# Kernel optimization log

Measured on AMD Instinct MI355X. Metric: run time of the kernel, lower is better.

The kernel has to match this reference:

```python
import jax, jax.numpy as jnp
from jax import lax
import numpy as np

T, C_IN, H, W = 32, 64, 128, 128
C_OUT, KH, KW = 128, 5, 5
H_OUT, W_OUT = H - KH + 1, W - KW + 1  # 124, 124
K_WINNERS = 256
LR_PLUS, LR_MINUS = 0.004, -0.003
LOWER, UPPER = 0.0, 1.0


def setup_inputs() -> dict:
    key = jax.random.key(0)
    k1, k2, k3, k4, k5, k6 = jax.random.split(key, 6)
    input_spikes = (jax.random.uniform(k1, (T, C_IN, H, W)) < 0.1).astype(jnp.float32)
    output_spikes = (jax.random.uniform(k2, (T, C_OUT, H_OUT, W_OUT)) < 0.05).astype(jnp.float32)
    weight = jax.random.uniform(k3, (C_OUT, C_IN, KH, KW), dtype=jnp.float32)
    f = jax.random.randint(k4, (K_WINNERS,), 0, C_OUT, dtype=jnp.int32)
    r = jax.random.randint(k5, (K_WINNERS,), 0, H_OUT, dtype=jnp.int32)
    c = jax.random.randint(k6, (K_WINNERS,), 0, W_OUT, dtype=jnp.int32)
    winners = jnp.stack([f, r, c], axis=1)  # [K, 3]
    return {"input_spikes": input_spikes, "output_spikes": output_spikes,
            "weight": weight, "winners": winners}


def reference(input_spikes, output_spikes, weight, winners):
    # latencies: sum spikes over time
    in_lat = jnp.sum(input_spikes, axis=0)    # [C_in, H, W]
    out_lat = jnp.sum(output_spikes, axis=0)  # [C_out, H_out, W_out]

    # gather per-winner input patches [K, C_in, kh, kw]
    def patch(rc):
        return lax.dynamic_slice(in_lat, (0, rc[0], rc[1]), (C_IN, KH, KW))
    patches = jax.vmap(patch)(winners[:, 1:])

    out_vals = out_lat[winners[:, 0], winners[:, 1], winners[:, 2]]  # [K]
    pair = patches >= out_vals[:, None, None, None]                  # [K, C_in, kh, kw]
    lr_vals = jnp.where(pair, LR_PLUS, LR_MINUS).astype(weight.dtype)

    # sequential scatter: later winners overwrite earlier ones (matches torch loop)
    def step(lr, inp):
        idx, val = inp
        return lr.at[idx].set(val), None
    lr, _ = lax.scan(step, jnp.zeros_like(weight), (winners[:, 0], lr_vals))

    stab = (weight - LOWER) * (UPPER - weight)  # use_stabilizer=True
    new_w = weight + lr * stab
    return jnp.clip(new_w, LOWER, UPPER)
```

## Files before the change

### kernel.cpp

```cpp
#include <hip/hip_runtime.h>

#define T 32
#define C_IN 64
#define H 128
#define W 128
#define C_OUT 128
#define KH 5
#define KW 5
#define H_OUT 124
#define W_OUT 124
#define K_WINNERS 256
#define LR_PLUS 0.004f
#define LR_MINUS -0.003f

#define BLOCKS_PER_F 5
#define BLOCK 320

__global__ __launch_bounds__(BLOCK) void stdp_fused(
        const float* __restrict__ in_spikes,
        const float* __restrict__ out_spikes,
        const float* __restrict__ weight,
        const int* __restrict__ winners,
        float* __restrict__ out) {
    __shared__ int s_k;
    __shared__ float s_part[T];
    __shared__ float s_outval;

    const int f = blockIdx.x / BLOCKS_PER_F;
    const int tid = threadIdx.x;

    if (tid == 0) s_k = -1;
    __syncthreads();
    if (tid < K_WINNERS && winners[tid * 3] == f)
        atomicMax(&s_k, tid);
    __syncthreads();
    const int k = s_k;

    int r0 = 0, c0 = 0;
    if (k >= 0) {
        r0 = winners[k * 3 + 1];
        c0 = winners[k * 3 + 2];
        if (tid < T) {
            s_part[tid] = out_spikes[(size_t)tid * (C_OUT * H_OUT * W_OUT)
                                     + (size_t)f * (H_OUT * W_OUT)
                                     + (size_t)r0 * W_OUT + c0];
        }
    }
    __syncthreads();
    if (k >= 0 && tid == 0) {
        float v = 0.0f;
        #pragma unroll
        for (int t = 0; t < T; ++t) v += s_part[t];
        s_outval = v;
    }
    __syncthreads();

    const int rem = (blockIdx.x % BLOCKS_PER_F) * BLOCK + tid;
    const int idx = f * (C_IN * KH * KW) + rem;
    float w = weight[idx];
    float res;
    if (k < 0) {
        res = w;
    } else {
        const int ci = rem / (KH * KW);
        const int p  = rem % (KH * KW);
        const int r  = r0 + p / KW;
        const int c  = c0 + p % KW;
        const float* ptr = in_spikes + (size_t)ci * (H * W) + (size_t)r * W + c;
        float sum = 0.0f;
        #pragma unroll
        for (int t = 0; t < T; ++t)
            sum += ptr[(size_t)t * (C_IN * H * W)];
        float lr = (sum >= s_outval) ? LR_PLUS : LR_MINUS;
        res = w + lr * w * (1.0f - w);
    }
    out[idx] = fminf(fmaxf(res, 0.0f), 1.0f);
}

extern "C" void kernel_launch(void* const* d_in, const int* in_sizes, int n_in,
                              void* d_out, int out_size, void* d_ws, size_t ws_size,
                              hipStream_t stream) {
    const float* in_spikes  = (const float*)d_in[0];
    const float* out_spikes = (const float*)d_in[1];
    const float* weight     = (const float*)d_in[2];
    const int*   winners    = (const int*)d_in[3];
    float* out = (float*)d_out;

    stdp_fused<<<C_OUT * BLOCKS_PER_F, BLOCK, 0, stream>>>(
        in_spikes, out_spikes, weight, winners, out);
}
```

Before: 365.2 us.

## Precompute input latencies with a dense vectorized time-sum kernel before applying STDP

Adds a separate kernel that sums input spikes over all time steps for the whole input tensor into workspace, using float4 loads. The update kernel then reads one precomputed latency per weight element instead of doing 32 strided gathers. This turns a latency-bound scattered gather into one coalesced streaming pass. The cost is reading the entire input tensor, including regions no winner uses, plus a second kernel launch and a workspace buffer.

```diff
diff --git a/kernel.cpp b/kernel.cpp
--- a/kernel.cpp
+++ b/kernel.cpp
@@ -13,11 +13,28 @@
 #define LR_PLUS 0.004f
 #define LR_MINUS -0.003f
 
+#define LAT_ELEMS (C_IN * H * W)
+#define LAT_VEC4  (LAT_ELEMS / 4)
+#define SUM_BLOCK 256
+#define SUM_GRID  (LAT_VEC4 / SUM_BLOCK)
+
+__global__ __launch_bounds__(SUM_BLOCK) void sum_over_t(
+        const float4* __restrict__ in4, float4* __restrict__ lat4) {
+    const int i = blockIdx.x * SUM_BLOCK + threadIdx.x;
+    float4 s = make_float4(0.f, 0.f, 0.f, 0.f);
+    #pragma unroll
+    for (int t = 0; t < T; ++t) {
+        float4 v = in4[(size_t)t * LAT_VEC4 + i];
+        s.x += v.x; s.y += v.y; s.z += v.z; s.w += v.w;
+    }
+    lat4[i] = s;
+}
+
 #define BLOCKS_PER_F 5
 #define BLOCK 320
 
-__global__ __launch_bounds__(BLOCK) void stdp_fused(
-        const float* __restrict__ in_spikes,
+__global__ __launch_bounds__(BLOCK) void stdp_apply(
+        const float* __restrict__ lat,
         const float* __restrict__ out_spikes,
         const float* __restrict__ weight,
         const int* __restrict__ winners,
@@ -66,11 +83,7 @@
         const int p  = rem % (KH * KW);
         const int r  = r0 + p / KW;
         const int c  = c0 + p % KW;
-        const float* ptr = in_spikes + (size_t)ci * (H * W) + (size_t)r * W + c;
-        float sum = 0.0f;
-        #pragma unroll
-        for (int t = 0; t < T; ++t)
-            sum += ptr[(size_t)t * (C_IN * H * W)];
+        const float sum = lat[(size_t)ci * (H * W) + (size_t)r * W + c];
         float lr = (sum >= s_outval) ? LR_PLUS : LR_MINUS;
         res = w + lr * w * (1.0f - w);
     }
@@ -84,8 +97,10 @@
     const float* out_spikes = (const float*)d_in[1];
     const float* weight     = (const float*)d_in[2];
     const int*   winners    = (const int*)d_in[3];
-    float* out = (float*)d_out;
+    float* lat = (float*)d_ws;
 
-    stdp_fused<<<C_OUT * BLOCKS_PER_F, BLOCK, 0, stream>>>(
-        in_spikes, out_spikes, weight, winners, out);
+    sum_over_t<<<SUM_GRID, SUM_BLOCK, 0, stream>>>(
+        (const float4*)in_spikes, (float4*)lat);
+    stdp_apply<<<C_OUT * BLOCKS_PER_F, BLOCK, 0, stream>>>(
+        lat, out_spikes, weight, winners, (float*)d_out);
 }
```

Result: no change. 362.8 us (-0.7%).
